# Kernel tuning notes

Measured on AMD Instinct MI355X. Metric: run time of the kernel, lower is better.

## Reference

```python
import jax, jax.numpy as jnp
import numpy as np

N = 128        # n_neurons == neuron_dim (required by einsum 'bdn,ijn')
IN_FEAT = 4608  # grid_size**2 * embed_dim_doubled = 9 * 512
B = 32          # batch(4) * num_candidates(8)


def setup_inputs() -> dict:
    key = jax.random.key(0)
    ks = jax.random.split(key, 8)
    s_in = 1.0 / np.sqrt(IN_FEAT)
    s_d = 1.0 / np.sqrt(N)
    return {
        "x": jax.random.normal(ks[0], (B, IN_FEAT), jnp.float32),
        "input_proj_w": jax.random.uniform(ks[1], (N, IN_FEAT), jnp.float32, -s_in, s_in),
        "input_proj_b": jax.random.uniform(ks[2], (N,), jnp.float32, -s_in, s_in),
        "neuron_states": jax.random.normal(ks[3], (N, N), jnp.float32),
        "edge_vectors": jax.random.normal(ks[4], (N, N, N), jnp.float32),
        "recreate_w": jax.random.uniform(ks[5], (IN_FEAT, N), jnp.float32, -s_d, s_d),
        "recreate_b": jnp.zeros((IN_FEAT,), jnp.float32),
        "score_w": jax.random.uniform(ks[6], (1, N), jnp.float32, -s_d, s_d),
        "score_b": jnp.zeros((1,), jnp.float32),
        "grid_size": 3,
        "num_candidates": 8,
        "n_steps": 2,
    }


def reference(x, input_proj_w, input_proj_b, neuron_states, edge_vectors,
              recreate_w, recreate_b, score_w, score_b,
              grid_size, num_candidates, n_steps):
    bc = x.shape[0]                                   # batch * num_candidates
    embed_dim_doubled = x.shape[1] // (grid_size ** 2)
    n = neuron_states.shape[0]                        # == neuron_dim

    x_t = x @ input_proj_w.T + input_proj_b          # (B, d)
    # neuron_states: (n, d) -> states: (B, d, n), input added per feature channel
    states = neuron_states.T[None, :, :] + x_t[:, :, None]
    mask = 1.0 - jnp.eye(n, dtype=x.dtype)            # (n, n), no self term

    for _ in range(n_steps):
        # (B,d,n) x (n,n,n) -> (B,d,i,j): the O(B*d*n^2) intermediate
        T = jnp.einsum('bdn,ijn->bdij', states, edge_vectors)
        messages = jnp.einsum('bdij,bdn->bdi', T, states)  # (B, d, n)
        # literal broadcast of mask (1,n,n) against (B,d,n); valid since d==n
        messages = messages * mask[None, :, :]
        states = jax.nn.relu(messages)                     # (B, d, n)

    out = states[:, :, -1]                                 # (B, d)
    recreation = out @ recreate_w.T + recreate_b           # (B, IN_FEAT)
    scores = out @ score_w.T + score_b                     # (B, 1)

    bsz = bc // num_candidates
    recreation = recreation.reshape(bsz, num_candidates, grid_size ** 2, embed_dim_doubled)
    scores = scores.reshape(bsz, num_candidates)
    return recreation, scores
```

## Files before the change

### kernel.cpp

```cpp
#include <hip/hip_runtime.h>


#define KQ 1152

__device__ __forceinline__ float wave_reduce64(float v) {
#pragma unroll
  for (int m = 32; m >= 1; m >>= 1) v += __shfl_xor(v, m);
  return v;
}
__device__ __forceinline__ float wave_reduce32(float v) {
#pragma unroll
  for (int m = 16; m >= 1; m >>= 1) v += __shfl_xor(v, m);
  return v;
}

#define WS_EJT 0
#define WS_E 16384
#define WS_EJ127 16512
#define WS_XT 16640
#define WS_OBD 20736

__global__ __launch_bounds__(256) void k1_pre(const float* __restrict__ ev,
                                              const float* __restrict__ x,
                                              const float* __restrict__ ipw,
                                              const float* __restrict__ ipb,
                                              float* __restrict__ ws) {
  int tid = threadIdx.x, blk = blockIdx.x;
  if (blk < 128) {
    __shared__ __align__(16) float4 sarr[256];
    int i = blk;
    int n4 = tid & 31, jg = tid >> 5;
    const float4* ev4 = (const float4*)ev;
    float4 acc = make_float4(0.f, 0.f, 0.f, 0.f);
#pragma unroll
    for (int jj = 0; jj < 16; ++jj) {
      int j = jg * 16 + jj;
      float4 v = ev4[i * 4096 + j * 32 + n4];
      acc.x += v.x; acc.y += v.y; acc.z += v.z; acc.w += v.w;
    }
    sarr[tid] = acc;
    __syncthreads();
    if (tid < 32) {
      float4 s = sarr[tid];
#pragma unroll
      for (int k = 1; k < 8; ++k) {
        float4 v = sarr[tid + 32 * k];
        s.x += v.x; s.y += v.y; s.z += v.z; s.w += v.w;
      }
      float* EJT = ws + WS_EJT;
      int n0 = tid * 4;
      EJT[(n0 + 0) * 128 + i] = s.x;
      EJT[(n0 + 1) * 128 + i] = s.y;
      EJT[(n0 + 2) * 128 + i] = s.z;
      EJT[(n0 + 3) * 128 + i] = s.w;
      if (i == 127) *(float4*)(ws + WS_EJ127 + n0) = s;
      float p = s.x + s.y + s.z + s.w;
      p = wave_reduce32(p);
      if (tid == 0) (ws + WS_E)[i] = p;
    }
  } else {
    int gw = (blk - 128) * 4 + (tid >> 6);
    int lane = tid & 63;
    int b0 = (gw >> 6) << 1, d0 = (gw & 63) << 1;
    const float4* x4 = (const float4*)x;
    const float4* w4 = (const float4*)ipw;
    float a00 = 0.f, a01 = 0.f, a10 = 0.f, a11 = 0.f;
#pragma unroll 6
    for (int kq = lane; kq < KQ; kq += 64) {
      float4 xa = x4[b0 * KQ + kq];
      float4 xb = x4[(b0 + 1) * KQ + kq];
      float4 wa = w4[d0 * KQ + kq];
      float4 wb = w4[(d0 + 1) * KQ + kq];
      a00 += xa.x * wa.x + xa.y * wa.y + xa.z * wa.z + xa.w * wa.w;
      a01 += xa.x * wb.x + xa.y * wb.y + xa.z * wb.z + xa.w * wb.w;
      a10 += xb.x * wa.x + xb.y * wa.y + xb.z * wa.z + xb.w * wa.w;
      a11 += xb.x * wb.x + xb.y * wb.y + xb.z * wb.z + xb.w * wb.w;
    }
    a00 = wave_reduce64(a00);
    a01 = wave_reduce64(a01);
    a10 = wave_reduce64(a10);
    a11 = wave_reduce64(a11);
    if (lane == 0) {
      float* xt = ws + WS_XT;
      xt[b0 * 128 + d0] = a00 + ipb[d0];
      xt[b0 * 128 + d0 + 1] = a01 + ipb[d0 + 1];
      xt[(b0 + 1) * 128 + d0] = a10 + ipb[d0];
      xt[(b0 + 1) * 128 + d0 + 1] = a11 + ipb[d0 + 1];
    }
  }
}

__global__ __launch_bounds__(256) void k2_brain(const float* __restrict__ ns,
                                                float* __restrict__ ws) {
  __shared__ float nscol[128], xts[32], at2[2][128], Atf[128];
  __shared__ float csum_s;
  int tid = threadIdx.x, d = blockIdx.x;
  if (tid < 128) nscol[tid] = ns[tid * 128 + d];
  else if (tid < 160) xts[tid - 128] = (ws + WS_XT)[(tid - 128) * 128 + d];
  __syncthreads();
  {
    int i = tid & 127, h = tid >> 7;
    const float* EJTp = ws + WS_EJT + h * 64 * 128 + i;
    const float* nsr = &nscol[h * 64];
    float a = 0.f;
#pragma unroll 8
    for (int n = 0; n < 64; ++n) a += EJTp[n * 128] * nsr[n];
    at2[h][i] = a;
  }
  if (tid < 64) {
    float cl = nscol[tid] + nscol[tid + 64];
    cl = wave_reduce64(cl);
    if (tid == 0) csum_s = cl;
  }
  __syncthreads();
  if (tid < 128) Atf[tid] = at2[0][tid] + at2[1][tid];
  __syncthreads();
  int wv = tid >> 6, l = tid & 63;
  float a0 = Atf[l], a1 = Atf[l + 64];
  float e0 = (ws + WS_E)[l], e1 = (ws + WS_E)[l + 64];
  float q0 = (ws + WS_EJ127)[l], q1 = (ws + WS_EJ127)[l + 64];
  float csum = csum_s;
  bool z0 = (l == d), z1 = (l + 64 == d);
  float* obd = ws + WS_OBD;
#pragma unroll
  for (int bb = 0; bb < 8; ++bb) {
    int b = wv * 8 + bb;
    float t = xts[b];
    float s0s = csum + 128.f * t;
    float v0 = s0s * (a0 + t * e0);
    float v1 = s0s * (a1 + t * e1);
    v0 = z0 ? 0.f : fmaxf(v0, 0.f);
    v1 = z1 ? 0.f : fmaxf(v1, 0.f);
    float sig = wave_reduce64(v0 + v1);
    float y = wave_reduce64(q0 * v0 + q1 * v1);
    if (l == 0) {
      float m2 = sig * y;
      if (d == 127) m2 = 0.f;
      obd[b * 128 + d] = fmaxf(m2, 0.f);
    }
  }
}

__global__ __launch_bounds__(256) void k3_proj(const float* __restrict__ rw,
                                               const float* __restrict__ rb,
                                               const float* __restrict__ sw,
                                               const float* __restrict__ sb,
                                               const float* __restrict__ ws,
                                               float* __restrict__ out) {
  const float* obd = ws + WS_OBD;
  int tid = threadIdx.x;
  int blk = blockIdx.x;
  if (blk < 144) {
    __shared__ __align__(16) float rwlds[32 * 136];
    __shared__ float obdT[128 * 33];
    int f0 = blk * 32;
    const float4* rw4 = (const float4*)rw;
#pragma unroll
    for (int it = 0; it < 4; ++it) {
      int q = tid + 256 * it;
      int f = q >> 5, n4 = q & 31;
      *(float4*)&rwlds[f * 136 + n4 * 4] = rw4[f0 * 32 + q];
    }
#pragma unroll
    for (int it = 0; it < 16; ++it) {
      int q = tid + 256 * it;
      int b = q >> 7, dd = q & 127;
      obdT[dd * 33 + b] = obd[q];
    }
    __syncthreads();
    int f = tid >> 3, bg = tid & 7;
    float acc[4] = {0.f, 0.f, 0.f, 0.f};
#pragma unroll 4
    for (int d = 0; d < 128; ++d) {
      float w = rwlds[f * 136 + d];
#pragma unroll
      for (int k = 0; k < 4; ++k) acc[k] += w * obdT[d * 33 + bg * 4 + k];
    }
    float bias = rb[f0 + f];
#pragma unroll
    for (int k = 0; k < 4; ++k) out[(bg * 4 + k) * 4608 + f0 + f] = acc[k] + bias;
  } else {
    int b = tid >> 3, l8 = tid & 7;
    float acc = 0.f;
    for (int d = l8; d < 128; d += 8) acc += obd[b * 128 + d] * sw[d];
    acc += __shfl_xor(acc, 1);
    acc += __shfl_xor(acc, 2);
    acc += __shfl_xor(acc, 4);
    if (l8 == 0) out[147456 + b] = acc + sb[0];
  }
}

extern "C" void kernel_launch(void* const* d_in, const int* in_sizes, int n_in,
                              void* d_out, int out_size, void* d_ws, size_t ws_size,
                              hipStream_t stream) {
  const float* x   = (const float*)d_in[0];
  const float* ipw = (const float*)d_in[1];
  const float* ipb = (const float*)d_in[2];
  const float* ns  = (const float*)d_in[3];
  const float* ev  = (const float*)d_in[4];
  const float* rw  = (const float*)d_in[5];
  const float* rb  = (const float*)d_in[6];
  const float* sw  = (const float*)d_in[7];
  const float* sb  = (const float*)d_in[8];
  float* out = (float*)d_out;
  float* ws = (float*)d_ws;

  k1_pre<<<384, 256, 0, stream>>>(ev, x, ipw, ipb, ws);
  k2_brain<<<128, 256, 0, stream>>>(ns, ws);
  k3_proj<<<145, 256, 0, stream>>>(rw, rb, sw, sb, ws, out);
}
```

Baseline: 99.23 us.

## Fuse three kernels into one persistent launch with atomic-counter inter-stage barriers

```diff
diff --git a/kernel.cpp b/kernel.cpp
--- a/kernel.cpp
+++ b/kernel.cpp
@@ -19,15 +19,21 @@
 #define WS_EJ127 16512
 #define WS_XT 16640
 #define WS_OBD 20736
-
-__global__ __launch_bounds__(256) void k1_pre(const float* __restrict__ ev,
-                                              const float* __restrict__ x,
-                                              const float* __restrict__ ipw,
-                                              const float* __restrict__ ipb,
-                                              float* __restrict__ ws) {
+#define WS_CTR 24832
+
+__global__ __launch_bounds__(256, 4) void brain_all(
+    const float* __restrict__ ev, const float* __restrict__ x,
+    const float* __restrict__ ipw, const float* __restrict__ ipb,
+    const float* __restrict__ ns, const float* __restrict__ rw,
+    const float* __restrict__ rb, const float* __restrict__ sw,
+    const float* __restrict__ sb, float* __restrict__ ws,
+    float* __restrict__ out) {
+  __shared__ __align__(16) float smem[8576];
   int tid = threadIdx.x, blk = blockIdx.x;
+  unsigned* ctr = (unsigned*)(ws + WS_CTR);
+
   if (blk < 128) {
-    __shared__ __align__(16) float4 sarr[256];
+    float4* sarr = (float4*)smem;
     int i = blk;
     int n4 = tid & 31, jg = tid >> 5;
     const float4* ev4 = (const float4*)ev;
@@ -58,14 +64,17 @@
       p = wave_reduce32(p);
       if (tid == 0) (ws + WS_E)[i] = p;
     }
-  } else {
+    __syncthreads();
+    if (tid == 0)
+      __hip_atomic_fetch_add(ctr, 1u, __ATOMIC_RELEASE, __HIP_MEMORY_SCOPE_AGENT);
+  } else if (blk < 384) {
     int gw = (blk - 128) * 4 + (tid >> 6);
     int lane = tid & 63;
     int b0 = (gw >> 6) << 1, d0 = (gw & 63) << 1;
     const float4* x4 = (const float4*)x;
     const float4* w4 = (const float4*)ipw;
     float a00 = 0.f, a01 = 0.f, a10 = 0.f, a11 = 0.f;
-#pragma unroll 6
+#pragma unroll 4
     for (int kq = lane; kq < KQ; kq += 64) {
       float4 xa = x4[b0 * KQ + kq];
       float4 xb = x4[(b0 + 1) * KQ + kq];
@@ -87,73 +96,71 @@
       xt[(b0 + 1) * 128 + d0] = a10 + ipb[d0];
       xt[(b0 + 1) * 128 + d0 + 1] = a11 + ipb[d0 + 1];
     }
-  }
-}
-
-__global__ __launch_bounds__(256) void k2_brain(const float* __restrict__ ns,
-                                                float* __restrict__ ws) {
-  __shared__ float nscol[128], xts[32], at2[2][128], Atf[128];
-  __shared__ float csum_s;
-  int tid = threadIdx.x, d = blockIdx.x;
-  if (tid < 128) nscol[tid] = ns[tid * 128 + d];
-  else if (tid < 160) xts[tid - 128] = (ws + WS_XT)[(tid - 128) * 128 + d];
-  __syncthreads();
-  {
-    int i = tid & 127, h = tid >> 7;
-    const float* EJTp = ws + WS_EJT + h * 64 * 128 + i;
-    const float* nsr = &nscol[h * 64];
-    float a = 0.f;
+    __syncthreads();
+    if (tid == 0)
+      __hip_atomic_fetch_add(ctr, 1u, __ATOMIC_RELEASE, __HIP_MEMORY_SCOPE_AGENT);
+  } else if (blk < 512) {
+    float* nscol = smem;
+    float* xts = smem + 128;
+    float* at2 = smem + 160;
+    float* Atf = smem + 416;
+    float* csum_s = smem + 544;
+    int d = blk - 384;
+    if (tid < 128) nscol[tid] = ns[tid * 128 + d];
+    if (tid == 0) {
+      while (__hip_atomic_load(ctr, __ATOMIC_ACQUIRE, __HIP_MEMORY_SCOPE_AGENT) < 384u)
+        __builtin_amdgcn_s_sleep(1);
+    }
+    __syncthreads();
+    if (tid >= 128 && tid < 160) xts[tid - 128] = (ws + WS_XT)[(tid - 128) * 128 + d];
+    {
+      int i = tid & 127, h = tid >> 7;
+      const float* EJTp = ws + WS_EJT + h * 64 * 128 + i;
+      const float* nsr = &nscol[h * 64];
+      float a = 0.f;
 #pragma unroll 8
-    for (int n = 0; n < 64; ++n) a += EJTp[n * 128] * nsr[n];
-    at2[h][i] = a;
-  }
-  if (tid < 64) {
-    float cl = nscol[tid] + nscol[tid + 64];
-    cl = wave_reduce64(cl);
-    if (tid == 0) csum_s = cl;
-  }
-  __syncthreads();
-  if (tid < 128) Atf[tid] = at2[0][tid] + at2[1][tid];
-  __syncthreads();
-  int wv = tid >> 6, l = tid & 63;
-  float a0 = Atf[l], a1 = Atf[l + 64];
-  float e0 = (ws + WS_E)[l], e1 = (ws + WS_E)[l + 64];
-  float q0 = (ws + WS_EJ127)[l], q1 = (ws + WS_EJ127)[l + 64];
-  float csum = csum_s;
-  bool z0 = (l == d), z1 = (l + 64 == d);
-  float* obd = ws + WS_OBD;
-#pragma unroll
-  for (int bb = 0; bb < 8; ++bb) {
-    int b = wv * 8 + bb;
-    float t = xts[b];
-    float s0s = csum + 128.f * t;
-    float v0 = s0s * (a0 + t * e0);
-    float v1 = s0s * (a1 + t * e1);
-    v0 = z0 ? 0.f : fmaxf(v0, 0.f);
-    v1 = z1 ? 0.f : fmaxf(v1, 0.f);
-    float sig = wave_reduce64(v0 + v1);
-    float y = wave_reduce64(q0 * v0 + q1 * v1);
-    if (l == 0) {
-      float m2 = sig * y;
-      if (d == 127) m2 = 0.f;
-      obd[b * 128 + d] = fmaxf(m2, 0.f);
-    }
-  }
-}
-
-__global__ __launch_bounds__(256) void k3_proj(const float* __restrict__ rw,
-                                               const float* __restrict__ rb,
-                                               const float* __restrict__ sw,
-                                               const float* __restrict__ sb,
-                                               const float* __restrict__ ws,
-                                               float* __restrict__ out) {
-  const float* obd = ws + WS_OBD;
-  int tid = threadIdx.x;
-  int blk = blockIdx.x;
-  if (blk < 144) {
-    __shared__ __align__(16) float rwlds[32 * 136];
-    __shared__ float obdT[128 * 33];
-    int f0 = blk * 32;
+      for (int n = 0; n < 64; ++n) a += EJTp[n * 128] * nsr[n];
+      at2[h * 128 + i] = a;
+    }
+    if (tid < 64) {
+      float cl = nscol[tid] + nscol[tid + 64];
+      cl = wave_reduce64(cl);
+      if (tid == 0) *csum_s = cl;
+    }
+    __syncthreads();
+    if (tid < 128) Atf[tid] = at2[tid] + at2[128 + tid];
+    __syncthreads();
+    int wv = tid >> 6, l = tid & 63;
+    float a0 = Atf[l], a1 = Atf[l + 64];
+    float e0 = (ws + WS_E)[l], e1 = (ws + WS_E)[l + 64];
+    float q0 = (ws + WS_EJ127)[l], q1 = (ws + WS_EJ127)[l + 64];
+    float csum = *csum_s;
+    bool z0 = (l == d), z1 = (l + 64 == d);
+    float* obd = ws + WS_OBD;
+#pragma unroll
+    for (int bb = 0; bb < 8; ++bb) {
+      int b = wv * 8 + bb;
+      float t = xts[b];
+      float s0s = csum + 128.f * t;
+      float v0 = s0s * (a0 + t * e0);
+      float v1 = s0s * (a1 + t * e1);
+      v0 = z0 ? 0.f : fmaxf(v0, 0.f);
+      v1 = z1 ? 0.f : fmaxf(v1, 0.f);
+      float sig = wave_reduce64(v0 + v1);
+      float y = wave_reduce64(q0 * v0 + q1 * v1);
+      if (l == 0) {
+        float m2 = sig * y;
+        if (d == 127) m2 = 0.f;
+        obd[b * 128 + d] = fmaxf(m2, 0.f);
+      }
+    }
+    __syncthreads();
+    if (tid == 0)
+      __hip_atomic_fetch_add(ctr + 1, 1u, __ATOMIC_RELEASE, __HIP_MEMORY_SCOPE_AGENT);
+  } else if (blk < 656) {
+    float* rwlds = smem;
+    float* obdT = smem + 4352;
+    int f0 = (blk - 512) * 32;
     const float4* rw4 = (const float4*)rw;
 #pragma unroll
     for (int it = 0; it < 4; ++it) {
@@ -161,6 +168,12 @@
       int f = q >> 5, n4 = q & 31;
       *(float4*)&rwlds[f * 136 + n4 * 4] = rw4[f0 * 32 + q];
     }
+    if (tid == 0) {
+      while (__hip_atomic_load(ctr + 1, __ATOMIC_ACQUIRE, __HIP_MEMORY_SCOPE_AGENT) < 128u)
+        __builtin_amdgcn_s_sleep(1);
+    }
+    __syncthreads();
+    const float* obd = ws + WS_OBD;
 #pragma unroll
     for (int it = 0; it < 16; ++it) {
       int q = tid + 256 * it;
@@ -180,6 +193,12 @@
 #pragma unroll
     for (int k = 0; k < 4; ++k) out[(bg * 4 + k) * 4608 + f0 + f] = acc[k] + bias;
   } else {
+    if (tid == 0) {
+      while (__hip_atomic_load(ctr + 1, __ATOMIC_ACQUIRE, __HIP_MEMORY_SCOPE_AGENT) < 128u)
+        __builtin_amdgcn_s_sleep(1);
+    }
+    __syncthreads();
+    const float* obd = ws + WS_OBD;
     int b = tid >> 3, l8 = tid & 7;
     float acc = 0.f;
     for (int d = l8; d < 128; d += 8) acc += obd[b * 128 + d] * sw[d];
@@ -205,7 +224,6 @@
   float* out = (float*)d_out;
   float* ws = (float*)d_ws;
 
-  k1_pre<<<384, 256, 0, stream>>>(ev, x, ipw, ipb, ws);
-  k2_brain<<<128, 256, 0, stream>>>(ns, ws);
-  k3_proj<<<145, 256, 0, stream>>>(rw, rb, sw, sb, ws, out);
-}
+  hipMemsetAsync((char*)d_ws + WS_CTR * sizeof(float), 0, 2 * sizeof(unsigned), stream);
+  brain_all<<<657, 256, 0, stream>>>(ev, x, ipw, ipb, ns, rw, rb, sw, sb, ws, out);
+}
```

Measured after the change: 177.5 us. +78.8%, slower.
